# Kernel optimization log

Hardware: AMD Instinct MI355X
Metric: run time of the kernel (lower is better)

The kernel has to match this reference:

```python
import jax, jax.numpy as jnp
import numpy as np

N_NODES = 50000
N_EDGES = 800000
N_GRAPHS = 64
D = 96              # input_dim = hidden_dim = output_dim
N_GIN = 4           # num_layers - 1 GINConv layers
N_HEADS = 5         # num_layers linear_prediction heads
BN_EPS = 1e-5


def setup_inputs() -> dict:
    key = jax.random.key(0)
    ks = jax.random.split(key, 16)
    s = 1.0 / np.sqrt(D)
    h = jax.random.normal(ks[0], (N_NODES, D), dtype=jnp.float32)
    src = jax.random.randint(ks[1], (N_EDGES,), 0, N_NODES, dtype=jnp.int32)
    dst = jax.random.randint(ks[2], (N_EDGES,), 0, N_NODES, dtype=jnp.int32)
    # sorted node->graph ids; deterministic so every graph is non-empty
    graph_ids = (jnp.arange(N_NODES, dtype=jnp.int32) * N_GRAPHS) // N_NODES
    return {
        "h": h,
        # GIN layer MLPs (num_mlp_layers=2): Linear -> BN -> ReLU -> Linear
        "gin_W1": jax.random.uniform(ks[3], (N_GIN, D, D), jnp.float32, -s, s),
        "gin_b1": jax.random.uniform(ks[4], (N_GIN, D), jnp.float32, -s, s),
        "gin_bn1_g": jnp.ones((N_GIN, D), jnp.float32),
        "gin_bn1_b": jnp.zeros((N_GIN, D), jnp.float32),
        "gin_W2": jax.random.uniform(ks[5], (N_GIN, D, D), jnp.float32, -s, s),
        "gin_b2": jax.random.uniform(ks[6], (N_GIN, D), jnp.float32, -s, s),
        # per-layer outer BatchNorm1d
        "bn_g": jnp.ones((N_GIN, D), jnp.float32),
        "bn_b": jnp.zeros((N_GIN, D), jnp.float32),
        # shared PReLU parameter (nn.PReLU default: 1 param, init 0.25)
        "prelu_a": jnp.full((1,), 0.25, jnp.float32),
        # linear_prediction heads
        "lin_W": jax.random.uniform(ks[7], (N_HEADS, D, D), jnp.float32, -s, s),
        "lin_b": jax.random.uniform(ks[8], (N_HEADS, D), jnp.float32, -s, s),
        "src": src,
        "dst": dst,
        "graph_ids": graph_ids,
    }


def _batchnorm(x, gamma, beta):
    # training-mode batch statistics over the node dim (biased variance, as torch)
    m = jnp.mean(x, axis=0)
    v = jnp.var(x, axis=0)
    return gamma * (x - m) * jax.lax.rsqrt(v + BN_EPS) + beta


def reference(h, gin_W1, gin_b1, gin_bn1_g, gin_bn1_b, gin_W2, gin_b2,
              bn_g, bn_b, prelu_a, lin_W, lin_b, src, dst, graph_ids):
    hidden_rep = [h]
    for l in range(N_GIN):
        # GINConv, sum aggregation, eps=0 (learn_eps=False): (1+eps)*h + sum_{j in N(i)} h_j
        agg = jax.ops.segment_sum(h[src], dst, num_segments=N_NODES)  # [N, D]
        z = h + agg
        # apply_func MLP: Linear -> BN -> ReLU -> Linear
        z = jax.nn.relu(_batchnorm(z @ gin_W1[l] + gin_b1[l], gin_bn1_g[l], gin_bn1_b[l]))
        z = z @ gin_W2[l] + gin_b2[l]
        # outer BatchNorm + PReLU
        z = _batchnorm(z, bn_g[l], bn_b[l])
        h = jnp.where(z >= 0, z, prelu_a * z)
        hidden_rep.append(h)
    # max graph pooling + per-layer linear heads (dropout = identity in eval)
    reps = []
    for l, hr in enumerate(hidden_rep):
        pooled = jax.ops.segment_max(hr, graph_ids, num_segments=N_GRAPHS)  # [B, D]
        reps.append(pooled @ lin_W[l] + lin_b[l])
    # layer_aggregation='cat': stack on dim=-1 then flatten -> [B, D * (N_GIN+1)]
    return jnp.stack(reps, axis=-1).reshape(N_GRAPHS, -1)
```

## Files before the change

### kernel.cpp

```cpp
#include <hip/hip_runtime.h>
#include <hip/hip_bf16.h>

#define N_NODES 50000
#define N_EDGES 800000
#define N_GRAPHS 64
#define D 96
#define N_GIN 4
#define BN_EPS 1e-5f
#define PCH 64
#define GEMM_GRID 782
#define LP 104
#define ELLCAP 72
#define SENT 50000
#define R1B 16667
#define R2B 33334

#define P1_BLOCKS 256
#define EPB 3125
#define BSH 8
#define BNODES 256
#define NBUCK 196
#define SPITCH 37

typedef __bf16 bf16;
typedef __bf16 bf16x8 __attribute__((ext_vector_type(8)));
typedef float f32x4 __attribute__((ext_vector_type(4)));
typedef unsigned short u16;
typedef unsigned int u32;
typedef unsigned short u16x8 __attribute__((ext_vector_type(8)));

__device__ inline unsigned enc(float f) {
    unsigned b = __float_as_uint(f);
    return (b & 0x80000000u) ? ~b : (b | 0x80000000u);
}
__device__ inline float dec(unsigned u) {
    return __uint_as_float((u & 0x80000000u) ? (u ^ 0x80000000u) : ~u);
}

__global__ void k_prolog(const float* __restrict__ h, bf16* __restrict__ hb,
                         bf16* __restrict__ hb1,
                         const float* __restrict__ W1, const float* __restrict__ W2,
                         bf16* __restrict__ wf, float* __restrict__ stats,
                         unsigned* __restrict__ pooledu) {
    int b = blockIdx.x;
    int tid = threadIdx.x;
    if (b < 2344) {
        int e = (b * 256 + tid) * 8;
        if (e >= N_NODES * D) return;
        float4 v0 = *(const float4*)(h + e);
        float4 v1 = *(const float4*)(h + e + 4);
        bf16x8 o;
        o[0] = (bf16)v0.x; o[1] = (bf16)v0.y; o[2] = (bf16)v0.z; o[3] = (bf16)v0.w;
        o[4] = (bf16)v1.x; o[5] = (bf16)v1.y; o[6] = (bf16)v1.z; o[7] = (bf16)v1.w;
        *(bf16x8*)(hb + e) = o;
    } else if (b < 2352) {
        int mat = b - 2344;
        const float* src = (mat < 4) ? (W1 + mat * D * D) : (W2 + (mat - 4) * D * D);
        bf16* dst = wf + mat * D * D;
        for (int p = tid; p < D * D; p += 256) {
            int f = p >> 9;
            int r = p & 511;
            int lane = r >> 3;
            int j = r & 7;
            int q = lane >> 4;
            int m16 = lane & 15;
            int nt = f / 3, ks = f % 3;
            int k = ks * 32 + q * 8 + j;
            int n = nt * 16 + m16;
            dst[p] = (bf16)src[k * D + n];
        }
    } else {
        int t = (b - 2352) * 256 + tid;
        if (t < N_GIN * 2 * 2 * D) stats[t] = 0.0f;
        if (t < 5 * N_GRAPHS * D) pooledu[t] = 0u;
        if (t < D) {
            hb[(size_t)SENT * D + t] = (bf16)0.0f;
            hb1[(size_t)SENT * D + t] = (bf16)0.0f;
        }
    }
}

__global__ void __launch_bounds__(256) k_part_pool(
        const int* __restrict__ src, const int* __restrict__ dst,
        u32* __restrict__ eo, u16* __restrict__ offs,
        const bf16* __restrict__ hb, unsigned* __restrict__ pooledu) {
    __shared__ u16 sdst[EPB + 3];
    __shared__ u16 ssrc[EPB + 3];
    __shared__ int hist[256];
    __shared__ int incl[256];
    int tid = threadIdx.x;
    if (blockIdx.x < P1_BLOCKS) {
        int e0 = blockIdx.x * EPB;
        hist[tid] = 0;
        __syncthreads();
        for (int i = tid; i < EPB; i += 256) {
            int d = dst[e0 + i];
            sdst[i] = (u16)d;
            ssrc[i] = (u16)src[e0 + i];
            atomicAdd(&hist[d >> BSH], 1);
        }
        __syncthreads();
        int v = hist[tid];
        incl[tid] = v;
        __syncthreads();
        for (int o = 1; o < 256; o <<= 1) {
            int t = (tid >= o) ? incl[tid - o] : 0;
            __syncthreads();
            incl[tid] += t;
            __syncthreads();
        }
        int ex = incl[tid] - v;
        if (tid <= NBUCK) offs[tid * P1_BLOCKS + blockIdx.x] = (u16)ex;
        hist[tid] = ex;
        __syncthreads();
        for (int i = tid; i < EPB; i += 256) {
            int d = sdst[i];
            int pos = atomicAdd(&hist[d >> BSH], 1);
            eo[e0 + pos] = ((u32)(d & (BNODES - 1)) << 16) | (u32)ssrc[i];
        }
    } else {
        int grp = (blockIdx.x - P1_BLOCKS) * 16 + (tid >> 4);
        int l = tid & 15;
        if (l >= 12) return;
        int g = grp / PCH, c = grp % PCH;
        int gs = (g * N_NODES + N_GRAPHS - 1) / N_GRAPHS;
        int ge = ((g + 1) * N_NODES + N_GRAPHS - 1) / N_GRAPHS;
        int len = ge - gs;
        int rs = gs + (len * c) / PCH;
        int re = gs + (len * (c + 1)) / PCH;
        const bf16x8* __restrict__ base = (const bf16x8*)hb;
        float m[8];
#pragma unroll
        for (int j = 0; j < 8; ++j) m[j] = -3e38f;
        int i = rs;
        for (; i + 2 <= re; i += 2) {
            bf16x8 r0 = base[i * 12 + l];
            bf16x8 r1 = base[(i + 1) * 12 + l];
#pragma unroll
            for (int j = 0; j < 8; ++j) m[j] = fmaxf(m[j], fmaxf((float)r0[j], (float)r1[j]));
        }
        if (i < re) {
            bf16x8 r = base[i * 12 + l];
#pragma unroll
            for (int j = 0; j < 8; ++j) m[j] = fmaxf(m[j], (float)r[j]);
        }
        unsigned* dstp = pooledu + (size_t)g * D + l * 8;
#pragma unroll
        for (int j = 0; j < 8; ++j) atomicMax(&dstp[j], enc(m[j]));
    }
}

__global__ void __launch_bounds__(256) k_ell_build(
        const u32* __restrict__ eo, const u16* __restrict__ offs,
        u16* __restrict__ ell, int* __restrict__ cnt) {
    __shared__ u32 sell32[BNODES * SPITCH];
    __shared__ int sc[3][BNODES];
    __shared__ int spk[BNODES];
    int tid = threadIdx.x;
    int b = blockIdx.x;
    for (int i = tid; i < BNODES * SPITCH; i += 256) sell32[i] = 0xC350C350u;
    sc[0][tid] = 0; sc[1][tid] = 0; sc[2][tid] = 0;
    __syncthreads();
    int beg = offs[b * P1_BLOCKS + tid];
    int end = offs[(b + 1) * P1_BLOCKS + tid];
    const u32* ep = eo + (size_t)tid * EPB;
    for (int i = beg; i < end; ++i) {
        u32 pk = ep[i];
        int dl = pk >> 16;
        int s = (int)(pk & 0xFFFF);
        int r = (s < R1B) ? 0 : ((s < R2B) ? 1 : 2);
        atomicAdd(&sc[r][dl], 1);
    }
    __syncthreads();
    {
        int c0 = sc[0][tid], c1 = sc[1][tid], c2 = sc[2][tid];
        int o1 = min((c0 + 7) & ~7, ELLCAP);
        int o2 = min(o1 + ((c1 + 7) & ~7), ELLCAP);
        int o3 = min(o2 + ((c2 + 7) & ~7), ELLCAP);
        spk[tid] = o1 | (o2 << 8) | (o3 << 16);
        sc[0][tid] = 0;
        sc[1][tid] = o1;
        sc[2][tid] = o2;
    }
    __syncthreads();
    u16* srows = (u16*)sell32;
    for (int i = beg; i < end; ++i) {
        u32 pk = ep[i];
        int dl = pk >> 16;
        int s = (int)(pk & 0xFFFF);
        int r = (s < R1B) ? 0 : ((s < R2B) ? 1 : 2);
        int pos = atomicAdd(&sc[r][dl], 1);
        int w = spk[dl];
        int lim = (r == 0) ? (w & 255) : ((r == 1) ? ((w >> 8) & 255) : ((w >> 16) & 255));
        if (pos < lim) srows[dl * (2 * SPITCH) + pos] = (u16)s;
    }
    __syncthreads();
    int node0 = b << BSH;
    int nn = min(BNODES, N_NODES - node0);
    if (tid < nn) cnt[node0 + tid] = spk[tid];
    u32* gell = (u32*)(ell + (size_t)node0 * ELLCAP);
    const int ROWW = ELLCAP / 2;
    for (int i = tid; i < nn * ROWW; i += 256) {
        int row = i / ROWW;
        int col = i - row * ROWW;
        gell[i] = sell32[row * SPITCH + col];
    }
}

__global__ void __launch_bounds__(256) k_agg_gemm(
        const bf16* __restrict__ prev, const int* __restrict__ cnt,
        const u16* __restrict__ ell, const bf16* __restrict__ Bf,
        const float* __restrict__ bias, bf16* __restrict__ Z,
        float* __restrict__ ssum, float* __restrict__ sssq) {
    __shared__ bf16 sA[4][16 * LP];
    __shared__ float sr1[4][D], sr2[4][D];
    int tid = threadIdx.x;
    int lane = tid & 63, wv = tid >> 6;
    int q = lane >> 4, m16 = lane & 15;
    int strip = blockIdx.x * 4 + wv;

    float psum[6], pssq[6];
#pragma unroll
    for (int f = 0; f < 6; ++f) { psum[f] = 0.0f; pssq[f] = 0.0f; }

    if (strip < 3125) {
        const bf16x8* __restrict__ base = (const bf16x8*)prev;
        int gl = m16;
        if (gl < 12) {
            u16x8 sentv;
#pragma unroll
            for (int j = 0; j < 8; ++j) sentv[j] = (u16)SENT;
#pragma unroll 1
            for (int rp = 0; rp < 2; ++rp) {
                int nA = strip * 16 + rp * 8 + q;
                int nB = nA + 4;
                float accA[8], accB[8];
                bf16x8 selfA = base[nA * 12 + gl];
                bf16x8 selfB = base[nB * 12 + gl];
#pragma unroll
                for (int j = 0; j < 8; ++j) { accA[j] = (float)selfA[j]; accB[j] = (float)selfB[j]; }
                int wA = cnt[nA];
                int wB = cnt[nB];
                const u16* rowA = ell + (size_t)nA * ELLCAP;
                const u16* rowB = ell + (size_t)nB * ELLCAP;
#pragma unroll 1
                for (int r = 0; r < 3; ++r) {
                    int sA_ = (r == 0) ? 0 : ((r == 1) ? (wA & 255) : ((wA >> 8) & 255));
                    int eA_ = (r == 0) ? (wA & 255) : ((r == 1) ? ((wA >> 8) & 255) : ((wA >> 16) & 255));
                    int sB_ = (r == 0) ? 0 : ((r == 1) ? (wB & 255) : ((wB >> 8) & 255));
                    int eB_ = (r == 0) ? (wB & 255) : ((r == 1) ? ((wB >> 8) & 255) : ((wB >> 16) & 255));
                    int LA = eA_ - sA_, LB = eB_ - sB_;
                    int dgr = (LA > LB) ? LA : LB;
                    const u16* epA = rowA + sA_;
                    const u16* epB = rowB + sB_;
                    for (int e = 0; e < dgr; e += 8) {
                        u16x8 ivA = sentv, ivB = sentv;
                        if (e < LA) ivA = *(const u16x8*)(epA + e);
                        if (e < LB) ivB = *(const u16x8*)(epB + e);
                        bf16x8 a0 = base[(int)ivA[0] * 12 + gl];
                        bf16x8 a1 = base[(int)ivA[1] * 12 + gl];
                        bf16x8 a2 = base[(int)ivA[2] * 12 + gl];
                        bf16x8 a3 = base[(int)ivA[3] * 12 + gl];
                        bf16x8 a4 = base[(int)ivA[4] * 12 + gl];
                        bf16x8 a5 = base[(int)ivA[5] * 12 + gl];
                        bf16x8 a6 = base[(int)ivA[6] * 12 + gl];
                        bf16x8 a7 = base[(int)ivA[7] * 12 + gl];
                        bf16x8 b0 = base[(int)ivB[0] * 12 + gl];
                        bf16x8 b1 = base[(int)ivB[1] * 12 + gl];
                        bf16x8 b2 = base[(int)ivB[2] * 12 + gl];
                        bf16x8 b3 = base[(int)ivB[3] * 12 + gl];
                        bf16x8 b4 = base[(int)ivB[4] * 12 + gl];
                        bf16x8 b5 = base[(int)ivB[5] * 12 + gl];
                        bf16x8 b6 = base[(int)ivB[6] * 12 + gl];
                        bf16x8 b7 = base[(int)ivB[7] * 12 + gl];
#pragma unroll
                        for (int j = 0; j < 8; ++j) {
                            accA[j] += (float)a0[j] + (float)a1[j] + (float)a2[j] + (float)a3[j]
                                     + (float)a4[j] + (float)a5[j] + (float)a6[j] + (float)a7[j];
                            accB[j] += (float)b0[j] + (float)b1[j] + (float)b2[j] + (float)b3[j]
                                     + (float)b4[j] + (float)b5[j] + (float)b6[j] + (float)b7[j];
                        }
                    }
                }
                bf16x8 oA, oB;
#pragma unroll
                for (int j = 0; j < 8; ++j) { oA[j] = (bf16)accA[j]; oB[j] = (bf16)accB[j]; }
                *(bf16x8*)&sA[wv][(rp * 8 + q) * LP + gl * 8] = oA;
                *(bf16x8*)&sA[wv][(rp * 8 + 4 + q) * LP + gl * 8] = oB;
            }
        }
        __asm__ volatile("s_waitcnt lgkmcnt(0)" ::: "memory");

        bf16x8 bfr[18];
#pragma unroll
        for (int f = 0; f < 18; ++f) bfr[f] = *(const bf16x8*)(Bf + (f * 64 + lane) * 8);

        bf16x8 a0 = *(const bf16x8*)&sA[wv][m16 * LP + q * 8];
        bf16x8 a1 = *(const bf16x8*)&sA[wv][m16 * LP + 32 + q * 8];
        bf16x8 a2 = *(const bf16x8*)&sA[wv][m16 * LP + 64 + q * 8];

#pragma unroll
        for (int f = 0; f < 6; ++f) {
            f32x4 acc = {0.0f, 0.0f, 0.0f, 0.0f};
            acc = __builtin_amdgcn_mfma_f32_16x16x32_bf16(a0, bfr[f * 3 + 0], acc, 0, 0, 0);
            acc = __builtin_amdgcn_mfma_f32_16x16x32_bf16(a1, bfr[f * 3 + 1], acc, 0, 0, 0);
            acc = __builtin_amdgcn_mfma_f32_16x16x32_bf16(a2, bfr[f * 3 + 2], acc, 0, 0, 0);
            int col = f * 16 + m16;
            float bvf = bias[col];
            bf16* zp = Z + (size_t)(strip * 16 + q * 4) * D + col;
#pragma unroll
            for (int i = 0; i < 4; ++i) {
                float v = acc[i] + bvf;
                zp[(size_t)i * D] = (bf16)v;
                psum[f] += v;
                pssq[f] += v * v;
            }
        }
    }
#pragma unroll
    for (int f = 0; f < 6; ++f) {
        float r = psum[f];
        r += __shfl_xor(r, 16);
        r += __shfl_xor(r, 32);
        float r2 = pssq[f];
        r2 += __shfl_xor(r2, 16);
        r2 += __shfl_xor(r2, 32);
        if (lane < 16) {
            sr1[wv][f * 16 + lane] = r;
            sr2[wv][f * 16 + lane] = r2;
        }
    }
    __syncthreads();
    int t = wv * 64 + lane;
    if (t < D) {
        atomicAdd(&ssum[t], sr1[0][t] + sr1[1][t] + sr1[2][t] + sr1[3][t]);
    } else if (t < 2 * D) {
        int u = t - D;
        atomicAdd(&sssq[u], sr2[0][u] + sr2[1][u] + sr2[2][u] + sr2[3][u]);
    }
}

__global__ void k_transform(const bf16* __restrict__ Z, const float* __restrict__ st,
                            const float* __restrict__ gamma, const float* __restrict__ beta,
                            const float* __restrict__ pa, bf16* __restrict__ O) {
    __shared__ float cs[D], ct[D];
    int t = threadIdx.x;
    if (t < D) {
        float m = st[t] * (1.0f / N_NODES);
        float v = st[D + t] * (1.0f / N_NODES) - m * m;
        float inv = rsqrtf(v + BN_EPS);
        float sc = gamma[t] * inv;
        cs[t] = sc;
        ct[t] = beta[t] - m * sc;
    }
    __syncthreads();
    int e = (blockIdx.x * 256 + t) * 8;
    if (e >= N_NODES * D) return;
    float alpha = pa[0];
    int c = e % D;
    bf16x8 z = *(const bf16x8*)(Z + e);
    bf16x8 o;
#pragma unroll
    for (int j = 0; j < 8; ++j) {
        float v = (float)z[j] * cs[c + j] + ct[c + j];
        o[j] = (bf16)(v >= 0.0f ? v : alpha * v);
    }
    *(bf16x8*)(O + e) = o;
}

__global__ void __launch_bounds__(256) k_gemm_fused(
        const bf16* __restrict__ A, const bf16* __restrict__ Bf,
        const float* __restrict__ st, const float* __restrict__ gamma,
        const float* __restrict__ beta, const float* __restrict__ bias,
        bf16* __restrict__ Z, float* __restrict__ ssum, float* __restrict__ sssq,
        unsigned* __restrict__ poolu) {
    __shared__ float cs[D], ct[D];
    __shared__ float sr1[4][D];
    __shared__ float sr2[4][D];
    __shared__ unsigned pmax[2 * D];
    int tid = threadIdx.x;
    if (tid < D) {
        float m = st[tid] * (1.0f / N_NODES);
        float v = st[D + tid] * (1.0f / N_NODES) - m * m;
        float inv = rsqrtf(v + BN_EPS);
        float sc = gamma[tid] * inv;
        cs[tid] = sc;
        ct[tid] = beta[tid] - m * sc;
    }
    if (tid < 2 * D) pmax[tid] = 0u;
    __syncthreads();

    int lane = tid & 63;
    int wv = tid >> 6;
    int w = (blockIdx.x * blockDim.x + tid) >> 6;
    int nw = (gridDim.x * blockDim.x) >> 6;
    int q = lane >> 4, m16 = lane & 15;
    int g0 = (int)(((long long)blockIdx.x * 64) * N_GRAPHS / N_NODES);

    float as_[3][8], at_[3][8];
#pragma unroll
    for (int ks = 0; ks < 3; ++ks)
#pragma unroll
        for (int j = 0; j < 8; ++j) {
            as_[ks][j] = cs[ks * 32 + q * 8 + j];
            at_[ks][j] = ct[ks * 32 + q * 8 + j];
        }

    bf16x8 bfr[18];
#pragma unroll
    for (int f = 0; f < 18; ++f) bfr[f] = *(const bf16x8*)(Bf + (f * 64 + lane) * 8);
    float bv[6];
#pragma unroll
    for (int f = 0; f < 6; ++f) bv[f] = bias[f * 16 + m16];
    float psum[6], pssq[6];
#pragma unroll
    for (int f = 0; f < 6; ++f) { psum[f] = 0.0f; pssq[f] = 0.0f; }

    const int NSTRIP = N_NODES / 16;
    for (int s = w; s < NSTRIP; s += nw) {
        const bf16* arow = A + (size_t)(s * 16 + m16) * D;
        bf16x8 z0 = *(const bf16x8*)(arow + q * 8);
        bf16x8 z1 = *(const bf16x8*)(arow + 32 + q * 8);
        bf16x8 z2 = *(const bf16x8*)(arow + 64 + q * 8);
        bf16x8 a0, a1, a2;
#pragma unroll
        for (int j = 0; j < 8; ++j) {
            a0[j] = (bf16)fmaxf(0.0f, (float)z0[j] * as_[0][j] + at_[0][j]);
            a1[j] = (bf16)fmaxf(0.0f, (float)z1[j] * as_[1][j] + at_[1][j]);
            a2[j] = (bf16)fmaxf(0.0f, (float)z2[j] * as_[2][j] + at_[2][j]);
        }
#pragma unroll
        for (int f = 0; f < 6; ++f) {
            f32x4 acc = {0.0f, 0.0f, 0.0f, 0.0f};
            acc = __builtin_amdgcn_mfma_f32_16x16x32_bf16(a0, bfr[f * 3 + 0], acc, 0, 0, 0);
            acc = __builtin_amdgcn_mfma_f32_16x16x32_bf16(a1, bfr[f * 3 + 1], acc, 0, 0, 0);
            acc = __builtin_amdgcn_mfma_f32_16x16x32_bf16(a2, bfr[f * 3 + 2], acc, 0, 0, 0);
            int col = f * 16 + m16;
            bf16* zp = Z + (size_t)(s * 16 + q * 4) * D + col;
#pragma unroll
            for (int i = 0; i < 4; ++i) {
                float v = acc[i] + bv[f];
                zp[(size_t)i * D] = (bf16)v;
                psum[f] += v;
                pssq[f] += v * v;
                int row = s * 16 + q * 4 + i;
                int g = (int)(((unsigned)row * 64u) / 50000u);
                int slot = g - g0;
                if (slot >= 0 && slot < 2)
                    atomicMax(&pmax[slot * D + col], enc(v));
            }
        }
    }
#pragma unroll
    for (int f = 0; f < 6; ++f) {
        float r = psum[f];
        r += __shfl_xor(r, 16);
        r += __shfl_xor(r, 32);
        float r2 = pssq[f];
        r2 += __shfl_xor(r2, 16);
        r2 += __shfl_xor(r2, 32);
        if (lane < 16) {
            sr1[wv][f * 16 + lane] = r;
            sr2[wv][f * 16 + lane] = r2;
        }
    }
    __syncthreads();
    int t = wv * 64 + lane;
    if (t < D) {
        atomicAdd(&ssum[t], sr1[0][t] + sr1[1][t] + sr1[2][t] + sr1[3][t]);
    } else if (t < 2 * D) {
        int u = t - D;
        atomicAdd(&sssq[u], sr2[0][u] + sr2[1][u] + sr2[2][u] + sr2[3][u]);
    }
    if (t < 2 * D) {
        int sl = t / D, c = t % D;
        int gg = g0 + sl;
        if (gg < N_GRAPHS && pmax[t] != 0u)
            atomicMax(&poolu[gg * D + c], pmax[t]);
    }
}

__global__ void k_heads(const unsigned* __restrict__ pooledu, const float* __restrict__ stats,
                        const float* __restrict__ bng, const float* __restrict__ bnb,
                        const float* __restrict__ pa, const float* __restrict__ W,
                        const float* __restrict__ B, float* __restrict__ out) {
    __shared__ float pv[D];
    int b = blockIdx.x;
    int l = b >> 6;
    int g = b & 63;
    int d = threadIdx.x;
    if (d < D) {
        float m = dec(pooledu[(size_t)(l * N_GRAPHS + g) * D + d]);
        if (l > 0) {
            int gl = l - 1;
            const float* st = stats + (gl * 2 + 1) * 2 * D;
            float mean = st[d] * (1.0f / N_NODES);
            float var = st[D + d] * (1.0f / N_NODES) - mean * mean;
            float inv = rsqrtf(var + BN_EPS);
            float s = bng[gl * D + d] * inv;
            float t = bnb[gl * D + d] - mean * s;
            float v = m * s + t;
            m = (v >= 0.0f) ? v : pa[0] * v;
        }
        pv[d] = m;
    }
    __syncthreads();
    if (d >= D) return;
    const float* w = W + (size_t)l * D * D;
    float acc = B[l * D + d];
    for (int k = 0; k < D; ++k) acc += pv[k] * w[k * D + d];
    out[g * (5 * D) + d * 5 + l] = acc;
}

extern "C" void kernel_launch(void* const* d_in, const int* in_sizes, int n_in,
                              void* d_out, int out_size, void* d_ws, size_t ws_size,
                              hipStream_t stream) {
    const float* h     = (const float*)d_in[0];
    const float* gW1   = (const float*)d_in[1];
    const float* gb1   = (const float*)d_in[2];
    const float* bn1g  = (const float*)d_in[3];
    const float* bn1b  = (const float*)d_in[4];
    const float* gW2   = (const float*)d_in[5];
    const float* gb2   = (const float*)d_in[6];
    const float* bng   = (const float*)d_in[7];
    const float* bnb   = (const float*)d_in[8];
    const float* prelu = (const float*)d_in[9];
    const float* linW  = (const float*)d_in[10];
    const float* linb  = (const float*)d_in[11];
    const int*   srcv  = (const int*)d_in[12];
    const int*   dstv  = (const int*)d_in[13];
    float* out = (float*)d_out;

    char* base = (char*)d_ws;
    size_t off = 0;
    auto carve = [&](size_t bytes) -> void* {
        void* p = base + off;
        off += (bytes + 255) & ~(size_t)255;
        return p;
    };
    const size_t HB = (size_t)N_NODES * D;
    bf16* hb0   = (bf16*)carve((HB + D) * 2);
    bf16* hb1   = (bf16*)carve((HB + D) * 2);
    bf16* zb    = (bf16*)carve(HB * 2);
    bf16* ab    = (bf16*)carve(HB * 2);
    bf16* wf    = (bf16*)carve(8 * D * D * 2);
    float* stats = (float*)carve(N_GIN * 2 * 2 * D * 4);
    int* cnt    = (int*)carve((size_t)N_NODES * 4);
    u16* ell    = (u16*)carve((size_t)N_NODES * ELLCAP * 2);
    u32* eo     = (u32*)carve((size_t)N_EDGES * 4);
    u16* offs   = (u16*)carve((size_t)(NBUCK + 1) * P1_BLOCKS * 2);
    unsigned* pooledu = (unsigned*)carve(5 * N_GRAPHS * D * 4);

    k_prolog<<<2472, 256, 0, stream>>>(h, hb0, hb1, gW1, gW2, wf, stats, pooledu);
    k_part_pool<<<P1_BLOCKS + N_GRAPHS * PCH / 16, 256, 0, stream>>>(
        srcv, dstv, eo, offs, hb0, pooledu);
    k_ell_build<<<NBUCK, 256, 0, stream>>>(eo, offs, ell, cnt);

    const bf16* prev = hb0;
    for (int l = 0; l < N_GIN; ++l) {
        float* st1 = stats + (l * 2 + 0) * 2 * D;
        float* st2 = stats + (l * 2 + 1) * 2 * D;
        if (l > 0) {
            float* stp = stats + ((l - 1) * 2 + 1) * 2 * D;
            k_transform<<<2344, 256, 0, stream>>>(ab, stp, bng + (l - 1) * D,
                                                  bnb + (l - 1) * D, prelu, hb1);
            prev = hb1;
        }
        k_agg_gemm<<<GEMM_GRID, 256, 0, stream>>>(prev, cnt, ell, wf + l * D * D,
                                                  gb1 + l * D, zb, st1, st1 + D);
        k_gemm_fused<<<GEMM_GRID, 256, 0, stream>>>(zb, wf + (4 + l) * D * D, st1,
                                                    bn1g + l * D, bn1b + l * D,
                                                    gb2 + l * D, ab, st2, st2 + D,
                                                    pooledu + (size_t)(l + 1) * N_GRAPHS * D);
    }
    k_heads<<<5 * N_GRAPHS, 128, 0, stream>>>(pooledu, stats, bng, bnb, prelu,
                                              linW, linb, out);
}
```

Before: 446.7 us.

## Split neighbor aggregation into per-source-range passes with fp32 accumulator buffer

```diff
diff --git a/kernel.cpp b/kernel.cpp
--- a/kernel.cpp
+++ b/kernel.cpp
@@ -9,6 +9,7 @@
 #define BN_EPS 1e-5f
 #define PCH 64
 #define GEMM_GRID 782
+#define PASS_GRID 1563
 #define LP 104
 #define ELLCAP 72
 #define SENT 50000
@@ -35,6 +36,12 @@
 }
 __device__ inline float dec(unsigned u) {
     return __uint_as_float((u & 0x80000000u) ? (u ^ 0x80000000u) : ~u);
+}
+__device__ __forceinline__ f32x4 ntload4(const f32x4* p) {
+    return __builtin_nontemporal_load(p);
+}
+__device__ __forceinline__ void ntstore4(f32x4* p, f32x4 v) {
+    __builtin_nontemporal_store(v, p);
 }
 
 __global__ void k_prolog(const float* __restrict__ h, bf16* __restrict__ hb,
@@ -207,11 +214,91 @@
     }
 }
 
+__global__ void __launch_bounds__(256) k_agg_pass(
+        const bf16* __restrict__ prev, const int* __restrict__ cnt,
+        const u16* __restrict__ ell, float* __restrict__ accf,
+        int range, int first) {
+    int tid = threadIdx.x;
+    int lane = tid & 63, wv = tid >> 6;
+    int q = lane >> 4, gl = lane & 15;
+    int w = blockIdx.x * 4 + wv;
+    if (w >= 6250 || gl >= 12) return;
+    const bf16x8* __restrict__ base = (const bf16x8*)prev;
+    int nA = w * 8 + q * 2;
+    int nB = nA + 1;
+    int wA = cnt[nA], wB = cnt[nB];
+    int sA_ = (range == 0) ? 0 : ((range == 1) ? (wA & 255) : ((wA >> 8) & 255));
+    int eA_ = (range == 0) ? (wA & 255) : ((range == 1) ? ((wA >> 8) & 255) : ((wA >> 16) & 255));
+    int sB_ = (range == 0) ? 0 : ((range == 1) ? (wB & 255) : ((wB >> 8) & 255));
+    int eB_ = (range == 0) ? (wB & 255) : ((range == 1) ? ((wB >> 8) & 255) : ((wB >> 16) & 255));
+    int LA = eA_ - sA_, LB = eB_ - sB_;
+    int dgr = (LA > LB) ? LA : LB;
+    float accA[8], accB[8];
+    if (first) {
+        bf16x8 selfA = base[nA * 12 + gl];
+        bf16x8 selfB = base[nB * 12 + gl];
+#pragma unroll
+        for (int j = 0; j < 8; ++j) { accA[j] = (float)selfA[j]; accB[j] = (float)selfB[j]; }
+    } else {
+#pragma unroll
+        for (int j = 0; j < 8; ++j) { accA[j] = 0.0f; accB[j] = 0.0f; }
+    }
+    u16x8 sentv;
+#pragma unroll
+    for (int j = 0; j < 8; ++j) sentv[j] = (u16)SENT;
+    const u16* epA = ell + (size_t)nA * ELLCAP + sA_;
+    const u16* epB = ell + (size_t)nB * ELLCAP + sB_;
+    for (int e = 0; e < dgr; e += 8) {
+        u16x8 ivA = sentv, ivB = sentv;
+        if (e < LA) ivA = *(const u16x8*)(epA + e);
+        if (e < LB) ivB = *(const u16x8*)(epB + e);
+        bf16x8 a0 = base[(int)ivA[0] * 12 + gl];
+        bf16x8 a1 = base[(int)ivA[1] * 12 + gl];
+        bf16x8 a2 = base[(int)ivA[2] * 12 + gl];
+        bf16x8 a3 = base[(int)ivA[3] * 12 + gl];
+        bf16x8 a4 = base[(int)ivA[4] * 12 + gl];
+        bf16x8 a5 = base[(int)ivA[5] * 12 + gl];
+        bf16x8 a6 = base[(int)ivA[6] * 12 + gl];
+        bf16x8 a7 = base[(int)ivA[7] * 12 + gl];
+        bf16x8 b0 = base[(int)ivB[0] * 12 + gl];
+        bf16x8 b1 = base[(int)ivB[1] * 12 + gl];
+        bf16x8 b2 = base[(int)ivB[2] * 12 + gl];
+        bf16x8 b3 = base[(int)ivB[3] * 12 + gl];
+        bf16x8 b4 = base[(int)ivB[4] * 12 + gl];
+        bf16x8 b5 = base[(int)ivB[5] * 12 + gl];
+        bf16x8 b6 = base[(int)ivB[6] * 12 + gl];
+        bf16x8 b7 = base[(int)ivB[7] * 12 + gl];
+#pragma unroll
+        for (int j = 0; j < 8; ++j) {
+            accA[j] += (float)a0[j] + (float)a1[j] + (float)a2[j] + (float)a3[j]
+                     + (float)a4[j] + (float)a5[j] + (float)a6[j] + (float)a7[j];
+            accB[j] += (float)b0[j] + (float)b1[j] + (float)b2[j] + (float)b3[j]
+                     + (float)b4[j] + (float)b5[j] + (float)b6[j] + (float)b7[j];
+        }
+    }
+    f32x4* pA = (f32x4*)(accf + (size_t)nA * D + gl * 8);
+    f32x4* pB = (f32x4*)(accf + (size_t)nB * D + gl * 8);
+    f32x4 vA0 = {accA[0], accA[1], accA[2], accA[3]};
+    f32x4 vA1 = {accA[4], accA[5], accA[6], accA[7]};
+    f32x4 vB0 = {accB[0], accB[1], accB[2], accB[3]};
+    f32x4 vB1 = {accB[4], accB[5], accB[6], accB[7]};
+    if (!first) {
+        f32x4 oA0 = ntload4(pA), oA1 = ntload4(pA + 1);
+        f32x4 oB0 = ntload4(pB), oB1 = ntload4(pB + 1);
+        vA0 += oA0;
+        vA1 += oA1;
+        vB0 += oB0;
+        vB1 += oB1;
+    }
+    ntstore4(pA, vA0); ntstore4(pA + 1, vA1);
+    ntstore4(pB, vB0); ntstore4(pB + 1, vB1);
+}
+
 __global__ void __launch_bounds__(256) k_agg_gemm(
         const bf16* __restrict__ prev, const int* __restrict__ cnt,
-        const u16* __restrict__ ell, const bf16* __restrict__ Bf,
-        const float* __restrict__ bias, bf16* __restrict__ Z,
-        float* __restrict__ ssum, float* __restrict__ sssq) {
+        const u16* __restrict__ ell, const float* __restrict__ accf,
+        const bf16* __restrict__ Bf, const float* __restrict__ bias,
+        bf16* __restrict__ Z, float* __restrict__ ssum, float* __restrict__ sssq) {
     __shared__ bf16 sA[4][16 * LP];
     __shared__ float sr1[4][D], sr2[4][D];
     int tid = threadIdx.x;
@@ -234,52 +321,46 @@
             for (int rp = 0; rp < 2; ++rp) {
                 int nA = strip * 16 + rp * 8 + q;
                 int nB = nA + 4;
-                float accA[8], accB[8];
-                bf16x8 selfA = base[nA * 12 + gl];
-                bf16x8 selfB = base[nB * 12 + gl];
-#pragma unroll
-                for (int j = 0; j < 8; ++j) { accA[j] = (float)selfA[j]; accB[j] = (float)selfB[j]; }
                 int wA = cnt[nA];
                 int wB = cnt[nB];
-                const u16* rowA = ell + (size_t)nA * ELLCAP;
-                const u16* rowB = ell + (size_t)nB * ELLCAP;
-#pragma unroll 1
-                for (int r = 0; r < 3; ++r) {
-                    int sA_ = (r == 0) ? 0 : ((r == 1) ? (wA & 255) : ((wA >> 8) & 255));
-                    int eA_ = (r == 0) ? (wA & 255) : ((r == 1) ? ((wA >> 8) & 255) : ((wA >> 16) & 255));
-                    int sB_ = (r == 0) ? 0 : ((r == 1) ? (wB & 255) : ((wB >> 8) & 255));
-                    int eB_ = (r == 0) ? (wB & 255) : ((r == 1) ? ((wB >> 8) & 255) : ((wB >> 16) & 255));
-                    int LA = eA_ - sA_, LB = eB_ - sB_;
-                    int dgr = (LA > LB) ? LA : LB;
-                    const u16* epA = rowA + sA_;
-                    const u16* epB = rowB + sB_;
-                    for (int e = 0; e < dgr; e += 8) {
-                        u16x8 ivA = sentv, ivB = sentv;
-                        if (e < LA) ivA = *(const u16x8*)(epA + e);
-                        if (e < LB) ivB = *(const u16x8*)(epB + e);
-                        bf16x8 a0 = base[(int)ivA[0] * 12 + gl];
-                        bf16x8 a1 = base[(int)ivA[1] * 12 + gl];
-                        bf16x8 a2 = base[(int)ivA[2] * 12 + gl];
-                        bf16x8 a3 = base[(int)ivA[3] * 12 + gl];
-                        bf16x8 a4 = base[(int)ivA[4] * 12 + gl];
-                        bf16x8 a5 = base[(int)ivA[5] * 12 + gl];
-                        bf16x8 a6 = base[(int)ivA[6] * 12 + gl];
-                        bf16x8 a7 = base[(int)ivA[7] * 12 + gl];
-                        bf16x8 b0 = base[(int)ivB[0] * 12 + gl];
-                        bf16x8 b1 = base[(int)ivB[1] * 12 + gl];
-                        bf16x8 b2 = base[(int)ivB[2] * 12 + gl];
-                        bf16x8 b3 = base[(int)ivB[3] * 12 + gl];
-                        bf16x8 b4 = base[(int)ivB[4] * 12 + gl];
-                        bf16x8 b5 = base[(int)ivB[5] * 12 + gl];
-                        bf16x8 b6 = base[(int)ivB[6] * 12 + gl];
-                        bf16x8 b7 = base[(int)ivB[7] * 12 + gl];
-#pragma unroll
-                        for (int j = 0; j < 8; ++j) {
-                            accA[j] += (float)a0[j] + (float)a1[j] + (float)a2[j] + (float)a3[j]
-                                     + (float)a4[j] + (float)a5[j] + (float)a6[j] + (float)a7[j];
-                            accB[j] += (float)b0[j] + (float)b1[j] + (float)b2[j] + (float)b3[j]
-                                     + (float)b4[j] + (float)b5[j] + (float)b6[j] + (float)b7[j];
-                        }
+                int sA_ = (wA >> 8) & 255, eA_ = (wA >> 16) & 255;
+                int sB_ = (wB >> 8) & 255, eB_ = (wB >> 16) & 255;
+                int LA = eA_ - sA_, LB = eB_ - sB_;
+                int dgr = (LA > LB) ? LA : LB;
+                const f32x4* pA4 = (const f32x4*)(accf + (size_t)nA * D + gl * 8);
+                const f32x4* pB4 = (const f32x4*)(accf + (size_t)nB * D + gl * 8);
+                f32x4 a40 = ntload4(pA4), a41 = ntload4(pA4 + 1);
+                f32x4 b40 = ntload4(pB4), b41 = ntload4(pB4 + 1);
+                float accA[8] = {a40[0], a40[1], a40[2], a40[3], a41[0], a41[1], a41[2], a41[3]};
+                float accB[8] = {b40[0], b40[1], b40[2], b40[3], b41[0], b41[1], b41[2], b41[3]};
+                const u16* epA = ell + (size_t)nA * ELLCAP + sA_;
+                const u16* epB = ell + (size_t)nB * ELLCAP + sB_;
+                for (int e = 0; e < dgr; e += 8) {
+                    u16x8 ivA = sentv, ivB = sentv;
+                    if (e < LA) ivA = *(const u16x8*)(epA + e);
+                    if (e < LB) ivB = *(const u16x8*)(epB + e);
+                    bf16x8 a0 = base[(int)ivA[0] * 12 + gl];
+                    bf16x8 a1 = base[(int)ivA[1] * 12 + gl];
+                    bf16x8 a2 = base[(int)ivA[2] * 12 + gl];
+                    bf16x8 a3 = base[(int)ivA[3] * 12 + gl];
+                    bf16x8 a4 = base[(int)ivA[4] * 12 + gl];
+                    bf16x8 a5 = base[(int)ivA[5] * 12 + gl];
+                    bf16x8 a6 = base[(int)ivA[6] * 12 + gl];
+                    bf16x8 a7 = base[(int)ivA[7] * 12 + gl];
+                    bf16x8 b0 = base[(int)ivB[0] * 12 + gl];
+                    bf16x8 b1 = base[(int)ivB[1] * 12 + gl];
+                    bf16x8 b2 = base[(int)ivB[2] * 12 + gl];
+                    bf16x8 b3 = base[(int)ivB[3] * 12 + gl];
+                    bf16x8 b4 = base[(int)ivB[4] * 12 + gl];
+                    bf16x8 b5 = base[(int)ivB[5] * 12 + gl];
+                    bf16x8 b6 = base[(int)ivB[6] * 12 + gl];
+                    bf16x8 b7 = base[(int)ivB[7] * 12 + gl];
+#pragma unroll
+                    for (int j = 0; j < 8; ++j) {
+                        accA[j] += (float)a0[j] + (float)a1[j] + (float)a2[j] + (float)a3[j]
+                                 + (float)a4[j] + (float)a5[j] + (float)a6[j] + (float)a7[j];
+                        accB[j] += (float)b0[j] + (float)b1[j] + (float)b2[j] + (float)b3[j]
+                                 + (float)b4[j] + (float)b5[j] + (float)b6[j] + (float)b7[j];
                     }
                 }
                 bf16x8 oA, oB;
@@ -543,6 +624,7 @@
     bf16* hb1   = (bf16*)carve((HB + D) * 2);
     bf16* zb    = (bf16*)carve(HB * 2);
     bf16* ab    = (bf16*)carve(HB * 2);
+    float* accf = (float*)carve(HB * 4);
     bf16* wf    = (bf16*)carve(8 * D * D * 2);
     float* stats = (float*)carve(N_GIN * 2 * 2 * D * 4);
     int* cnt    = (int*)carve((size_t)N_NODES * 4);
@@ -566,8 +648,11 @@
                                                   bnb + (l - 1) * D, prelu, hb1);
             prev = hb1;
         }
-        k_agg_gemm<<<GEMM_GRID, 256, 0, stream>>>(prev, cnt, ell, wf + l * D * D,
-                                                  gb1 + l * D, zb, st1, st1 + D);
+        k_agg_pass<<<PASS_GRID, 256, 0, stream>>>(prev, cnt, ell, accf, 0, 1);
+        k_agg_pass<<<PASS_GRID, 256, 0, stream>>>(prev, cnt, ell, accf, 1, 0);
+        k_agg_gemm<<<GEMM_GRID, 256, 0, stream>>>(prev, cnt, ell, accf,
+                                                  wf + l * D * D, gb1 + l * D,
+                                                  zb, st1, st1 + D);
         k_gemm_fused<<<GEMM_GRID, 256, 0, stream>>>(zb, wf + (4 + l) * D * D, st1,
                                                     bn1g + l * D, bn1b + l * D,
                                                     gb2 + l * D, ab, st2, st2 + D,
```

Result: slower. 516.3 us (+15.6%).
